# Performance work log

Hardware: AMD Instinct MI355X
Metric: run time of the kernel (lower is better)

## Reference

```python
import jax, jax.numpy as jnp
import numpy as np

MIN_DIST = 4
BASE_PRIMES = np.array([2, 3, 5, 7])  # A, C, G, U
# canonical pair prime products: AU=2*7=14, CG=3*5=15, GU=5*7=35


def nussinov(s):
    """Nussinov max-score non-crossing pairing: O(N^3) DP (vectorized per
    anti-diagonal) + stack-based traceback. s: [N,N] float64, symmetric, >=0.
    Returns symmetric 0/1 pair mask. Mirrors kirigami.nussinov (CPU numpy)."""
    N = s.shape[0]
    D = np.zeros((N, N))  # D[d, i] = dp[i, i+d]
    E = np.zeros((N, N))  # E[d, j] = dp[j-d, j]
    ar = np.arange(N)
    for d in range(1, N):
        m = N - d
        pair = (D[d - 2, 1:m + 1] if d >= 2 else 0.0) + s[ar[:m], ar[:m] + d]
        # split over k=i..j-1: dp[i,k] + dp[k+1,j] (k=i covers i-unpaired)
        split = (D[0:d, 0:m] + E[d - 1::-1, d:N]).max(axis=0)
        val = np.maximum(pair, split)
        D[d, :m] = val
        E[d, d:] = val
    dp = np.zeros((N, N))
    for d in range(1, N):
        dp[ar[:N - d], ar[:N - d] + d] = D[d, :N - d]
    eps = 1e-9
    pm = np.zeros((N, N))
    stack = [(0, N - 1)]
    while stack:
        i, j = stack.pop()
        if j <= i:
            continue
        v = dp[i, j]
        if v <= eps:
            continue
        if dp[i + 1, j] >= v - eps:
            stack.append((i + 1, j))
        elif s[i, j] > 0 and dp[i + 1, j - 1] + s[i, j] >= v - eps:
            pm[i, j] = pm[j, i] = 1.0
            stack.append((i + 1, j - 1))
        else:
            ks = np.arange(i, j)
            k = int(ks[np.argmax(dp[i, ks] + dp[ks + 1, j])])
            stack.append((i, k))
            stack.append((k + 1, j))
    return pm


def _premask(con, feat):
    """Symmetrize + remove sharp angles (tril(-4)+triu(4)) + canonical-pair mask."""
    c = con[0, 0]                      # [N, N]
    c = (c + c.T) * 0.5                # Symmetrize
    N = c.shape[0]
    idx = jnp.arange(N)
    dist_ok = jnp.abs(idx[:, None] - idx[None, :]) >= MIN_DIST  # RemoveSharp
    seq = feat[0, :4, :, 0]            # [4, N] one-hot base encoding
    primes = jnp.asarray(BASE_PRIMES)[jnp.argmax(seq, axis=0)]  # [N]
    prod = primes[:, None] * primes[None, :]
    canon = (prod == 14) | (prod == 15) | (prod == 35)          # Canonicalize
    return c * (dist_ok & canon)


def setup_inputs() -> dict:
    key = jax.random.key(0)
    k1, k2 = jax.random.split(key)
    N = 1024
    con = jax.random.uniform(k1, (1, 1, N, N), dtype=jnp.float32)
    feat = jax.random.normal(k2, (1, 16, N, N), dtype=jnp.float32)
    return {"con": con, "feat": feat}


def reference(con, feat):
    c = _premask(con, feat)
    # original: GPU->CPU numpy float64 DP, then mask back on device
    mask = nussinov(np.asarray(c, dtype=np.float64))
    out = c * jnp.asarray(mask, dtype=c.dtype)
    return out.reshape(con.shape)
```

## Files before the change

kernel.cpp:

```cpp
#include <hip/hip_runtime.h>

#define NN 1024
#define BT 32
#define TT 32
#define NTILES ((TT * (TT + 1)) / 2)

__device__ __forceinline__ double gload_cc(const double* p) {
    double v;
    asm volatile("global_load_dwordx2 %0, %1, off sc0 sc1" : "=v"(v) : "v"(p));
    return v;
}
__device__ __forceinline__ void gstore_cc(double* p, double v) {
    asm volatile("global_store_dwordx2 %0, %1, off sc0 sc1" :: "v"(p), "v"(v));
}
__device__ __forceinline__ void gstore_flag(int* p, int v) {
    asm volatile("global_store_dword %0, %1, off sc0 sc1" :: "v"(p), "v"(v));
}
#define VWAIT0 asm volatile("s_waitcnt vmcnt(0)" ::: "memory")

__device__ __forceinline__ void waitflag2(const int* f, int a0, int b0, int a1, int b1) {
    const int* p0 = &f[(a0 * TT + b0) << 4];
    const int* p1 = &f[(a1 * TT + b1) << 4];
    int it = 0;
    while (true) {
        int v0, v1;
        asm volatile("global_load_dword %0, %2, off sc0 sc1\n\t"
                     "global_load_dword %1, %3, off sc0 sc1\n\t"
                     "s_waitcnt vmcnt(0)"
                     : "=&v"(v0), "=&v"(v1)
                     : "v"(p0), "v"(p1));
        if (v0 & v1) break;
        if (it < 8) __builtin_amdgcn_s_sleep(1);
        else        __builtin_amdgcn_s_sleep(15);
        ++it;
    }
    asm volatile("" ::: "memory");
}
__device__ __forceinline__ void waitflag4(const int* f, int a0, int b0, int a1, int b1,
                                          int a2, int b2, int a3, int b3) {
    const int* p0 = &f[(a0 * TT + b0) << 4];
    const int* p1 = &f[(a1 * TT + b1) << 4];
    const int* p2 = &f[(a2 * TT + b2) << 4];
    const int* p3 = &f[(a3 * TT + b3) << 4];
    int it = 0;
    while (true) {
        int v0, v1, v2, v3;
        asm volatile("global_load_dword %0, %4, off sc0 sc1\n\t"
                     "global_load_dword %1, %5, off sc0 sc1\n\t"
                     "global_load_dword %2, %6, off sc0 sc1\n\t"
                     "global_load_dword %3, %7, off sc0 sc1\n\t"
                     "s_waitcnt vmcnt(0)"
                     : "=&v"(v0), "=&v"(v1), "=&v"(v2), "=&v"(v3)
                     : "v"(p0), "v"(p1), "v"(p2), "v"(p3));
        if (v0 & v1 & v2 & v3) break;
        if (it < 8) __builtin_amdgcn_s_sleep(1);
        else        __builtin_amdgcn_s_sleep(15);
        ++it;
    }
    asm volatile("" ::: "memory");
}
__device__ __forceinline__ void waitflag2_blk(const int* f, int a0, int b0, int a1, int b1) {
    if (threadIdx.x < 64) waitflag2(f, a0, b0, a1, b1);
    __syncthreads();
}
__device__ __forceinline__ void waitflag4_blk(const int* f, int a0, int b0, int a1, int b1,
                                              int a2, int b2, int a3, int b3) {
    if (threadIdx.x < 64) waitflag4(f, a0, b0, a1, b1, a2, b2, a3, b3);
    __syncthreads();
}

__global__ void primes_kernel(const float* __restrict__ feat, int* __restrict__ primes) {
    int i = blockIdx.x * blockDim.x + threadIdx.x;
    if (i < NN) {
        float best = feat[i * NN];
        int arg = 0;
        for (int ch = 1; ch < 4; ++ch) {
            float v = feat[ch * NN * NN + i * NN];
            if (v > best) { best = v; arg = ch; }
        }
        const int P[4] = {2, 3, 5, 7};
        primes[i] = P[arg];
    }
}

__global__ void prep_kernel(const float* __restrict__ con, const int* __restrict__ primes,
                            float* __restrict__ S, double* __restrict__ R,
                            double* __restrict__ C, float* __restrict__ out,
                            int* __restrict__ flags,
                            int* __restrict__ qi, int* __restrict__ qj,
                            int* __restrict__ qready, int* __restrict__ qctl) {
    int idx = blockIdx.x * blockDim.x + threadIdx.x;
    int i = idx >> 10;
    int j = idx & (NN - 1);
    float c = (con[idx] + con[j * NN + i]) * 0.5f;
    int prod = primes[i] * primes[j];
    bool canon = (prod == 14) | (prod == 15) | (prod == 35);
    int d = i - j; if (d < 0) d = -d;
    S[idx] = (canon && d >= 4) ? c : 0.0f;
    R[idx] = 0.0;
    C[idx] = 0.0;
    out[idx] = 0.0f;
    if (idx < TT * TT * 16) flags[idx] = 0;
    if (idx < 4096) qready[idx] = (idx == 0) ? 1 : 0;
    if (idx == 0) {
        qi[0] = 0; qj[0] = NN - 1;
        qctl[0] = 0;
        qctl[16] = 1;
        qctl[32] = 1;
    }
}

__global__ __launch_bounds__(256) void nuss_tiles_kernel(double* __restrict__ R,
                                                         double* __restrict__ C,
                                                         const float* __restrict__ S,
                                                         int* __restrict__ flags) {
    __shared__ double DJJc[32][33];
    __shared__ double Vtc[32][33];
    __shared__ __attribute__((aligned(16))) double Ast[32][34];
    __shared__ __attribute__((aligned(16))) double Bst[32][34];
    __shared__ double Pld[32][33];
    __shared__ float  Sld[32][32];
    __shared__ double edgeCol[33];

    int b = blockIdx.x, dd = 0;
    while (b >= TT - dd) { b -= TT - dd; ++dd; }
    const int I = b, J = b + dd;
    const int aI = I * BT, aJ = J * BT;
    const int tid = threadIdx.x;
    const int wid = tid >> 6;
    const int lane = tid & 63;
    const int r = lane >> 1;
    const int h = lane & 1;

    if (dd == 0) {
        #pragma unroll
        for (int w = 0; w < 4; ++w) {
            int idx = w * 256 + tid; int rr = idx >> 5, cc = idx & 31;
            Sld[rr][cc] = S[(aI + rr) * NN + aI + cc];
        }
        for (int idx = tid; idx < 32 * 33; idx += 256)
            ((double*)Vtc)[idx] = 0.0;
        __syncthreads();
        if (wid == 0) {
            double vrow[16];
            #pragma unroll
            for (int u = 0; u < 16; ++u) vrow[u] = 0.0;
            for (int s = 1; s <= 31; ++s) {
                int c = r + s;
                bool act = (c <= 31);
                double acc = 0.0;
                if (act) {
                    double t0 = 0.0, t1 = 0.0, t2 = 0.0, t3 = 0.0;
                    #pragma unroll
                    for (int u = 0; u < 16; u += 4) {
                        int k0 = h * 16 + u;
                        t0 = fmax(t0, vrow[u]     + Vtc[c][k0 + 1]);
                        t1 = fmax(t1, vrow[u + 1] + Vtc[c][k0 + 2]);
                        t2 = fmax(t2, vrow[u + 2] + Vtc[c][k0 + 3]);
                        t3 = fmax(t3, vrow[u + 3] + Vtc[c][k0 + 4]);
                    }
                    acc = fmax(fmax(t0, t1), fmax(t2, t3));
                }
                acc = fmax(acc, __shfl_xor(acc, 1));
                if (act) {
                    double best = fmax(acc, Vtc[c - 1][r + 1] + (double)Sld[r][c]);
                    if (h == 0) Vtc[c][r] = best;
                    #pragma unroll
                    for (int u = 0; u < 16; ++u)
                        if (h * 16 + u == c) vrow[u] = best;
                }
            }
        }
        __syncthreads();
        #pragma unroll
        for (int w = 0; w < 4; ++w) {
            int idx = w * 256 + tid; int rr = idx >> 5, cc = idx & 31;
            gstore_cc(&R[(aI + rr) * NN + aI + cc], Vtc[cc][rr]);
        }
        #pragma unroll
        for (int w = 0; w < 4; ++w) {
            int idx = w * 256 + tid; int cc = idx >> 5, rr = idx & 31;
            gstore_cc(&C[(aI + cc) * NN + aI + rr], Vtc[cc][rr]);
        }
        VWAIT0;
        __syncthreads();
        if (tid == 0) gstore_flag(&flags[(I * TT + I) << 4], 1);
        return;
    }

    const int nk = dd - 1;
    waitflag2_blk(flags, I, I, J, J);

    double ra[4], rb[4];
    double ec = 0.0, ve = 0.0;
    double asl[16];
    #pragma unroll
    for (int w = 0; w < 4; ++w) {
        int idx = w * 256 + tid; int cc = idx >> 5, mm = idx & 31;
        ra[w] = gload_cc(&C[(aJ + cc) * NN + aJ + mm]);
    }
    if (wid == 0) {
        #pragma unroll
        for (int u = 0; u < 16; ++u)
            asl[u] = gload_cc(&R[(aI + r) * NN + aI + h * 16 + u]);
        if (nk == 0) {
            if (lane < 33) ec = gload_cc(&R[(aI + lane) * NN + (aJ - 1)]);
            if (lane < 32) ve = gload_cc(&R[(aI + 32) * NN + aJ + lane]);
        }
    }
    #pragma unroll
    for (int w = 0; w < 4; ++w) {
        int idx = w * 256 + tid; int rr = idx >> 5, cc = idx & 31;
        Sld[rr][cc] = S[(aI + rr) * NN + aJ + cc];
    }
    for (int idx = tid; idx < 32 * 33; idx += 256)
        ((double*)Vtc)[idx] = 0.0;
    VWAIT0;
    #pragma unroll
    for (int w = 0; w < 4; ++w) {
        int idx = w * 256 + tid; int cc = idx >> 5, mm = idx & 31;
        DJJc[cc][mm] = ra[w];
    }
    if (tid < 32) DJJc[tid][32] = 0.0;
    double aslice[16];
    if (wid == 0) {
        #pragma unroll
        for (int u = 0; u < 16; ++u)
            aslice[u] = (h * 16 + u > r) ? asl[u] : -1.0e30;
    }
    __syncthreads();

    double P[16];
    #pragma unroll
    for (int x = 0; x < 16; ++x) P[x] = 0.0;
    const int rg = lane >> 3, cg = lane & 7;
    const int r4 = rg * 4, c4 = cg * 4;

    auto kkloop = [&]() {
        for (int kk = wid * 8; kk < wid * 8 + 8; ++kk) {
            double2 av0 = *(const double2*)&Ast[kk][r4];
            double2 av1 = *(const double2*)&Ast[kk][r4 + 2];
            double2 bv0 = *(const double2*)&Bst[kk][c4];
            double2 bv1 = *(const double2*)&Bst[kk][c4 + 2];
            P[0]  = fmax(P[0],  av0.x + bv0.x); P[1]  = fmax(P[1],  av0.x + bv0.y);
            P[2]  = fmax(P[2],  av0.x + bv1.x); P[3]  = fmax(P[3],  av0.x + bv1.y);
            P[4]  = fmax(P[4],  av0.y + bv0.x); P[5]  = fmax(P[5],  av0.y + bv0.y);
            P[6]  = fmax(P[6],  av0.y + bv1.x); P[7]  = fmax(P[7],  av0.y + bv1.y);
            P[8]  = fmax(P[8],  av1.x + bv0.x); P[9]  = fmax(P[9],  av1.x + bv0.y);
            P[10] = fmax(P[10], av1.x + bv1.x); P[11] = fmax(P[11], av1.x + bv1.y);
            P[12] = fmax(P[12], av1.y + bv0.x); P[13] = fmax(P[13], av1.y + bv0.y);
            P[14] = fmax(P[14], av1.y + bv1.x); P[15] = fmax(P[15], av1.y + bv1.y);
        }
    };
    auto proc = [&](int t1, int t2, bool last) {
        if (t2 >= 0) waitflag4_blk(flags, I, t1, t1, J, I, t2, t2, J);
        else         waitflag2_blk(flags, I, t1, t1, J);
        if (last && wid == 0) {
            if (lane < 33) ec = gload_cc(&R[(aI + lane) * NN + (aJ - 1)]);
            if (lane < 32) ve = gload_cc(&R[(aI + 32) * NN + aJ + lane]);
        }
        int k1 = t1 * BT;
        #pragma unroll
        for (int w = 0; w < 4; ++w) {
            int idx = w * 256 + tid; int rr = idx >> 5, kk = idx & 31;
            ra[w] = gload_cc(&R[(aI + rr) * NN + k1 + kk]);
            rb[w] = gload_cc(&C[(aJ + rr) * NN + k1 + 1 + kk]);
        }
        VWAIT0;
        #pragma unroll
        for (int w = 0; w < 4; ++w) {
            int idx = w * 256 + tid; int rr = idx >> 5, kk = idx & 31;
            Ast[kk][rr] = ra[w];
            Bst[kk][rr] = rb[w];
        }
        if (last && wid == 0) {
            if (lane < 33) edgeCol[lane] = ec;
            if (lane < 32) Vtc[lane][32] = ve;
        }
        __syncthreads();
        if (t2 >= 0) {
            int k2 = t2 * BT;
            #pragma unroll
            for (int w = 0; w < 4; ++w) {
                int idx = w * 256 + tid; int rr = idx >> 5, kk = idx & 31;
                ra[w] = gload_cc(&R[(aI + rr) * NN + k2 + kk]);
                rb[w] = gload_cc(&C[(aJ + rr) * NN + k2 + 1 + kk]);
            }
        }
        kkloop();
        if (t2 >= 0) {
            __syncthreads();
            VWAIT0;
            #pragma unroll
            for (int w = 0; w < 4; ++w) {
                int idx = w * 256 + tid; int rr = idx >> 5, kk = idx & 31;
                Ast[kk][rr] = ra[w];
                Bst[kk][rr] = rb[w];
            }
            __syncthreads();
            kkloop();
        }
        __syncthreads();
    };

    {
        int tl = (I + J) >> 1, tr = ((I + J) >> 1) + 1;
        int pend = -1;
        for (int q = 0; q < nk; ++q) {
            int t;
            if ((q & 1) == 0) { if (tl >= I + 1) t = tl--; else t = tr++; }
            else              { if (tr <= J - 1) t = tr++; else t = tl--; }
            if (pend < 0) { pend = t; continue; }
            int rp = (pend - I > J - pend) ? pend - I : J - pend;
            int rt = (t - I > J - t) ? t - I : J - t;
            if (rp == rt) { proc(pend, t, q == nk - 1); pend = -1; }
            else          { proc(pend, -1, false); pend = t; }
        }
        if (pend >= 0) proc(pend, -1, true);
    }

    if (nk > 0) {
        if (wid == 0) {
            #pragma unroll
            for (int x = 0; x < 4; ++x)
                #pragma unroll
                for (int y = 0; y < 4; ++y)
                    Pld[r4 + x][c4 + y] = P[x * 4 + y];
        }
        __syncthreads();
        if (wid == 1) {
            #pragma unroll
            for (int x = 0; x < 4; ++x)
                #pragma unroll
                for (int y = 0; y < 4; ++y)
                    Pld[r4 + x][c4 + y] = fmax(Pld[r4 + x][c4 + y], P[x * 4 + y]);
        }
        __syncthreads();
        if (wid == 2) {
            #pragma unroll
            for (int x = 0; x < 4; ++x)
                #pragma unroll
                for (int y = 0; y < 4; ++y)
                    Pld[r4 + x][c4 + y] = fmax(Pld[r4 + x][c4 + y], P[x * 4 + y]);
        }
        __syncthreads();
        if (wid == 3) {
            #pragma unroll
            for (int x = 0; x < 4; ++x)
                #pragma unroll
                for (int y = 0; y < 4; ++y)
                    Pld[r4 + x][c4 + y] = fmax(Pld[r4 + x][c4 + y], P[x * 4 + y]);
        }
        __syncthreads();
    } else {
        for (int idx = tid; idx < 32 * 33; idx += 256)
            ((double*)Pld)[idx] = 0.0;
        if (wid == 0) {
            if (lane < 33) edgeCol[lane] = ec;
            if (lane < 32) Vtc[lane][32] = ve;
        }
        __syncthreads();
    }

    if (wid == 0) {
        double vrow[16];
        #pragma unroll
        for (int u = 0; u < 16; ++u) vrow[u] = 0.0;

        double ecr = edgeCol[r];
        double ecp = edgeCol[r + 1];

        double tvA[16], qvA[16], tvB[16], qvB[16];
        double p1 = 0.0, shc = 0.0, shp = 0.0, erc = 0.0, erp = 0.0;

#define PREFB(TV, QV, SS)                                             \
    { int cc_ = (r + (SS) - 31) & 31;                                 \
      _Pragma("unroll")                                               \
      for (int u = 0; u < 16; ++u) {                                  \
          TV[u] = Vtc[cc_][h * 16 + u + 1];                           \
          QV[u] = DJJc[cc_][h * 16 + u + 1];                          \
      } }

#define STEPB(TV, QV, SS)                                             \
    { int c_ = r + (SS) - 31;                                         \
      bool act_ = ((unsigned)c_ < 32u);                               \
      int cc_ = c_ & 31;                                              \
      double er_  = Vtc[cc_][32];                                     \
      double dj0_ = DJJc[cc_][0];                                     \
      double pld_ = Pld[r][cc_];                                      \
      float  sld_ = Sld[r][cc_];                                      \
      shp = shc; erp = erc; erc = er_;                                \
      shc = __shfl_down(p1, 2);                                       \
      double acc_ = -1.0e30;                                          \
      if (act_) {                                                     \
          double t0_ = -1.0e30, t1_ = -1.0e30, t2_ = -1.0e30, t3_ = -1.0e30; \
          _Pragma("unroll")                                           \
          for (int u = 0; u < 16; u += 4) {                           \
              t0_ = fmax(t0_, aslice[u]     + TV[u]);                 \
              t1_ = fmax(t1_, aslice[u + 1] + TV[u + 1]);             \
              t2_ = fmax(t2_, aslice[u + 2] + TV[u + 2]);             \
              t3_ = fmax(t3_, aslice[u + 3] + TV[u + 3]);             \
          }                                                           \
          _Pragma("unroll")                                           \
          for (int u = 0; u < 16; u += 4) {                           \
              t0_ = fmax(t0_, vrow[u]     + QV[u]);                   \
              t1_ = fmax(t1_, vrow[u + 1] + QV[u + 1]);               \
              t2_ = fmax(t2_, vrow[u + 2] + QV[u + 2]);               \
              t3_ = fmax(t3_, vrow[u + 3] + QV[u + 3]);               \
          }                                                           \
          acc_ = fmax(fmax(t0_, t1_), fmax(t2_, t3_));                \
      }                                                               \
      acc_ = fmax(acc_, __shfl_xor(acc_, 1));                         \
      if (act_) {                                                     \
          double best_ = acc_;                                        \
          best_ = fmax(best_, (r == 31) ? erc : shc);                 \
          best_ = fmax(best_, ecr + dj0_);                            \
          best_ = fmax(best_, pld_);                                  \
          double pv_ = (c_ == 0) ? ecp : ((r == 31) ? erp : shp);     \
          best_ = fmax(best_, pv_ + (double)sld_);                    \
          if (h == 0) Vtc[c_][r] = best_;                             \
          _Pragma("unroll")                                           \
          for (int u = 0; u < 16; ++u)                                \
              if (h * 16 + u == c_) vrow[u] = best_;                  \
          p1 = best_;                                                 \
      } }

        PREFB(tvA, qvA, 0)
        for (int s2 = 0; s2 < 64; s2 += 2) {
            PREFB(tvB, qvB, s2 + 1)
            STEPB(tvA, qvA, s2)
            PREFB(tvA, qvA, s2 + 2)
            STEPB(tvB, qvB, s2 + 1)
        }
#undef PREFB
#undef STEPB
    }
    __syncthreads();

    #pragma unroll
    for (int w = 0; w < 4; ++w) {
        int idx = w * 256 + tid; int rr = idx >> 5, cc = idx & 31;
        gstore_cc(&R[(aI + rr) * NN + aJ + cc], Vtc[cc][rr]);
    }
    #pragma unroll
    for (int w = 0; w < 4; ++w) {
        int idx = w * 256 + tid; int cc = idx >> 5, rr = idx & 31;
        gstore_cc(&C[(aJ + cc) * NN + aI + rr], Vtc[cc][rr]);
    }
    VWAIT0;
    __syncthreads();
    if (tid == 0) gstore_flag(&flags[(I * TT + J) << 4], 1);
}

__global__ __launch_bounds__(256) void traceback_kernel(const double* __restrict__ R,
                                                        const double* __restrict__ C,
                                                        const float* __restrict__ S,
                                                        float* __restrict__ out,
                                                        int* __restrict__ qi,
                                                        int* __restrict__ qj,
                                                        int* __restrict__ qready,
                                                        int* __restrict__ qctl) {
    __shared__ double Rw[16][17];
    __shared__ float  Sw[16][17];
    __shared__ int sh_cmd, sh_i, sh_j;
    __shared__ double sred_v[4];
    __shared__ int sred_k[4];
    const double eps = 1e-9;
    const int tid = threadIdx.x;
    int* headp = qctl;
    int* tailp = qctl + 16;
    int* pendp = qctl + 32;

    int i = 0, j = 0; double v = 0.0;
    bool have = false;
    int ai = -(1 << 29), aj = 0;
    int myidx = -1;

    while (true) {
        if (tid == 0) {
            int cmd;
            int guard = 0;
            while (true) {
                if (!have) {
                    if (++guard > (1 << 22)) { cmd = -1; break; }
                    if (myidx < 0) myidx = atomicAdd(headp, 1);
                    int rdy = 0;
                    if (myidx < 4096)
                        rdy = __hip_atomic_load(&qready[myidx], __ATOMIC_RELAXED,
                                                __HIP_MEMORY_SCOPE_AGENT);
                    if (rdy) {
                        int ni, nj;
                        asm volatile("global_load_dword %0, %2, off sc0 sc1\n\t"
                                     "global_load_dword %1, %3, off sc0 sc1\n\t"
                                     "s_waitcnt vmcnt(0)"
                                     : "=&v"(ni), "=&v"(nj)
                                     : "v"(&qi[myidx]), "v"(&qj[myidx]));
                        myidx = -1;
                        i = ni; j = nj;
                        if (j <= i) { atomicAdd(pendp, -1); continue; }
                        v = R[i * NN + j];
                        if (v <= eps) { atomicAdd(pendp, -1); continue; }
                        have = true;
                        continue;
                    }
                    int pend = __hip_atomic_load(pendp, __ATOMIC_RELAXED,
                                                 __HIP_MEMORY_SCOPE_AGENT);
                    if (pend == 0) { cmd = -1; break; }
                    __builtin_amdgcn_s_sleep(2);
                    continue;
                }
                int u = i - ai, w = aj - j;
                if ((unsigned)u > 15u || (unsigned)w > 14u) { cmd = 1; break; }
                double a = Rw[u][w];
                if (a >= v - eps) {
                    ++i; v = a;
                    if (j <= i || v <= eps) { have = false; atomicAdd(pendp, -1); }
                    continue;
                }
                float sv = Sw[u][w];
                double b2 = Rw[u][w + 1];
                if (sv > 0.0f && b2 + (double)sv >= v - eps) {
                    out[i * NN + j] = sv; out[j * NN + i] = sv;
                    ++i; --j; v = b2;
                    if (j <= i || v <= eps) { have = false; atomicAdd(pendp, -1); }
                    continue;
                }
                cmd = 0; break;
            }
            sh_cmd = cmd; sh_i = i; sh_j = j;
        }
        __syncthreads();
        int cmd = sh_cmd;
        if (cmd < 0) break;

        if (cmd == 1) {
            int i0 = sh_i, j0 = sh_j;
            int di = tid >> 4, dj = tid & 15;
            int rr = i0 + 1 + di; if (rr > NN - 1) rr = NN - 1;
            int cc = j0 - dj;     if (cc < 0) cc = 0;
            Rw[di][dj] = R[rr * NN + cc];
            int sr = i0 + di;     if (sr > NN - 1) sr = NN - 1;
            Sw[di][dj] = S[sr * NN + cc];
            __syncthreads();
            if (tid == 0) { ai = i0; aj = j0; }
            continue;
        }

        const int si = sh_i, sj = sh_j;
        double bv = -1.0; int bk = 0x7fffffff;
        for (int k = si + tid; k < sj; k += 256) {
            double tv = R[si * NN + k] + C[sj * NN + k + 1];
            if (tv > bv) { bv = tv; bk = k; }
        }
        for (int off = 32; off; off >>= 1) {
            double ov = __shfl_down(bv, off);
            int    ok = __shfl_down(bk, off);
            if (ov > bv || (ov == bv && ok < bk)) { bv = ov; bk = ok; }
        }
        if ((tid & 63) == 0) { sred_v[tid >> 6] = bv; sred_k[tid >> 6] = bk; }
        __syncthreads();
        if (tid == 0) {
            double fv = sred_v[0]; int fk = sred_k[0];
            for (int w = 1; w < 4; ++w)
                if (sred_v[w] > fv || (sred_v[w] == fv && sred_k[w] < fk)) { fv = sred_v[w]; fk = sred_k[w]; }
            int slot = atomicAdd(tailp, 1);
            int rv = fk + 1;
            asm volatile("global_store_dword %0, %1, off sc0 sc1" :: "v"(&qi[slot]), "v"(rv));
            asm volatile("global_store_dword %0, %1, off sc0 sc1" :: "v"(&qj[slot]), "v"(sj));
            VWAIT0;
            atomicAdd(pendp, 1);
            VWAIT0;
            gstore_flag(&qready[slot], 1);
            j = fk;
            if (j <= i) { have = false; atomicAdd(pendp, -1); }
            else {
                v = R[i * NN + j];
                if (v <= eps) { have = false; atomicAdd(pendp, -1); }
                else have = true;
            }
        }
        __syncthreads();
    }
}

extern "C" void kernel_launch(void* const* d_in, const int* in_sizes, int n_in,
                              void* d_out, int out_size, void* d_ws, size_t ws_size,
                              hipStream_t stream) {
    const float* con  = (const float*)d_in[0];
    const float* feat = (const float*)d_in[1];
    float* out = (float*)d_out;

    char* ws = (char*)d_ws;
    double* R      = (double*)(ws);
    double* C      = (double*)(ws + (size_t)8  * 1024 * 1024);
    float*  S      = (float*) (ws + (size_t)16 * 1024 * 1024);
    int*    primes = (int*)   (ws + (size_t)20 * 1024 * 1024);
    int*    flags  = (int*)   (ws + (size_t)20 * 1024 * 1024 + 8192);
    char*   qbase  = ws + (size_t)20 * 1024 * 1024 + 128 * 1024;
    int*    qi     = (int*)(qbase);
    int*    qj     = (int*)(qbase + 16 * 1024);
    int*    qready = (int*)(qbase + 32 * 1024);
    int*    qctl   = (int*)(qbase + 48 * 1024);

    primes_kernel<<<(NN + 255) / 256, 256, 0, stream>>>(feat, primes);
    prep_kernel<<<(NN * NN) / 256, 256, 0, stream>>>(con, primes, S, R, C, out, flags,
                                                     qi, qj, qready, qctl);
    nuss_tiles_kernel<<<NTILES, 256, 0, stream>>>(R, C, S, flags);
    traceback_kernel<<<64, 256, 0, stream>>>(R, C, S, out, qi, qj, qready, qctl);
}
```

Before: 1.300 ms.

## Split tile wavefront recurrence across four waves with shared partial-max exchange

```diff
diff --git a/kernel.cpp b/kernel.cpp
--- a/kernel.cpp
+++ b/kernel.cpp
@@ -121,6 +121,7 @@
     __shared__ double Pld[32][33];
     __shared__ float  Sld[32][32];
     __shared__ double edgeCol[33];
+    __shared__ double Prt[2][4][32];
 
     int b = blockIdx.x, dd = 0;
     while (b >= TT - dd) { b -= TT - dd; ++dd; }
@@ -189,24 +190,27 @@
     }
 
     const int nk = dd - 1;
+    const int off = (wid & 1) * 16 + h * 8;
     waitflag2_blk(flags, I, I, J, J);
 
     double ra[4], rb[4];
     double ec = 0.0, ve = 0.0;
-    double asl[16];
+    double asl[8];
+    double ar1 = 0.0;
     #pragma unroll
     for (int w = 0; w < 4; ++w) {
         int idx = w * 256 + tid; int cc = idx >> 5, mm = idx & 31;
         ra[w] = gload_cc(&C[(aJ + cc) * NN + aJ + mm]);
     }
-    if (wid == 0) {
-        #pragma unroll
-        for (int u = 0; u < 16; ++u)
-            asl[u] = gload_cc(&R[(aI + r) * NN + aI + h * 16 + u]);
-        if (nk == 0) {
-            if (lane < 33) ec = gload_cc(&R[(aI + lane) * NN + (aJ - 1)]);
-            if (lane < 32) ve = gload_cc(&R[(aI + 32) * NN + aJ + lane]);
-        }
+    if (wid < 2) {
+        #pragma unroll
+        for (int u = 0; u < 8; ++u)
+            asl[u] = gload_cc(&R[(aI + r) * NN + aI + off + u]);
+    }
+    if (r < 31) ar1 = gload_cc(&R[(aI + r) * NN + aI + r + 1]);
+    if (wid == 0 && nk == 0) {
+        if (lane < 33) ec = gload_cc(&R[(aI + lane) * NN + (aJ - 1)]);
+        if (lane < 32) ve = gload_cc(&R[(aI + 32) * NN + aJ + lane]);
     }
     #pragma unroll
     for (int w = 0; w < 4; ++w) {
@@ -222,11 +226,18 @@
         DJJc[cc][mm] = ra[w];
     }
     if (tid < 32) DJJc[tid][32] = 0.0;
-    double aslice[16];
-    if (wid == 0) {
-        #pragma unroll
-        for (int u = 0; u < 16; ++u)
-            aslice[u] = (h * 16 + u > r) ? asl[u] : -1.0e30;
+    double slice8[8];
+    if (wid < 2) {
+        #pragma unroll
+        for (int u = 0; u < 8; ++u)
+            slice8[u] = (off + u > r + 1) ? asl[u] : -1.0e30;
+    } else {
+        #pragma unroll
+        for (int u = 0; u < 8; ++u) slice8[u] = 0.0;
+    }
+    if (wid == 0 && nk == 0) {
+        if (lane < 33) edgeCol[lane] = ec;
+        if (lane < 32) Vtc[lane][32] = ve;
     }
     __syncthreads();
 
@@ -355,85 +366,75 @@
     } else {
         for (int idx = tid; idx < 32 * 33; idx += 256)
             ((double*)Pld)[idx] = 0.0;
-        if (wid == 0) {
-            if (lane < 33) edgeCol[lane] = ec;
-            if (lane < 32) Vtc[lane][32] = ve;
-        }
-        __syncthreads();
-    }
-
-    if (wid == 0) {
-        double vrow[16];
-        #pragma unroll
-        for (int u = 0; u < 16; ++u) vrow[u] = 0.0;
-
+        __syncthreads();
+    }
+
+    {
+        const double* bsel = (wid < 2) ? &Vtc[0][0] : &DJJc[0][0];
         double ecr = edgeCol[r];
         double ecp = edgeCol[r + 1];
-
-        double tvA[16], qvA[16], tvB[16], qvB[16];
-        double p1 = 0.0, shc = 0.0, shp = 0.0, erc = 0.0, erp = 0.0;
-
-#define PREFB(TV, QV, SS)                                             \
-    { int cc_ = (r + (SS) - 31) & 31;                                 \
+        double pA[8], pB[8];
+        double p1 = 0.0, p2 = 0.0, shc = 0.0, shp = 0.0, erc = 0.0, erp = 0.0;
+
+#define PREFQ(PV, SS)                                                 \
+    { int cq_ = (r + (SS) - 31) & 31;                                 \
+      const double* bp_ = bsel + cq_ * 33 + off + 1;                  \
       _Pragma("unroll")                                               \
-      for (int u = 0; u < 16; ++u) {                                  \
-          TV[u] = Vtc[cc_][h * 16 + u + 1];                           \
-          QV[u] = DJJc[cc_][h * 16 + u + 1];                          \
-      } }
-
-#define STEPB(TV, QV, SS)                                             \
+      for (int u = 0; u < 8; ++u) PV[u] = bp_[u]; }
+
+#define STEPQ(PV, SS, BUF)                                            \
     { int c_ = r + (SS) - 31;                                         \
       bool act_ = ((unsigned)c_ < 32u);                               \
       int cc_ = c_ & 31;                                              \
+      double t0_ = fmax(slice8[0] + PV[0], slice8[1] + PV[1]);        \
+      double t1_ = fmax(slice8[2] + PV[2], slice8[3] + PV[3]);        \
+      double t2_ = fmax(slice8[4] + PV[4], slice8[5] + PV[5]);        \
+      double t3_ = fmax(slice8[6] + PV[6], slice8[7] + PV[7]);        \
+      double pa_ = fmax(fmax(t0_, t1_), fmax(t2_, t3_));              \
+      pa_ = fmax(pa_, __shfl_xor(pa_, 1));                            \
+      if (h == 0) Prt[BUF][wid][r] = pa_;                             \
+      __syncthreads();                                                \
+      double a0_ = Prt[BUF][0][r];                                    \
+      double a1_ = Prt[BUF][1][r];                                    \
+      double a2_ = Prt[BUF][2][r];                                    \
+      double a3_ = Prt[BUF][3][r];                                    \
       double er_  = Vtc[cc_][32];                                     \
       double dj0_ = DJJc[cc_][0];                                     \
       double pld_ = Pld[r][cc_];                                      \
       float  sld_ = Sld[r][cc_];                                      \
       shp = shc; erp = erc; erc = er_;                                \
       shc = __shfl_down(p1, 2);                                       \
-      double acc_ = -1.0e30;                                          \
-      if (act_) {                                                     \
-          double t0_ = -1.0e30, t1_ = -1.0e30, t2_ = -1.0e30, t3_ = -1.0e30; \
-          _Pragma("unroll")                                           \
-          for (int u = 0; u < 16; u += 4) {                           \
-              t0_ = fmax(t0_, aslice[u]     + TV[u]);                 \
-              t1_ = fmax(t1_, aslice[u + 1] + TV[u + 1]);             \
-              t2_ = fmax(t2_, aslice[u + 2] + TV[u + 2]);             \
-              t3_ = fmax(t3_, aslice[u + 3] + TV[u + 3]);             \
-          }                                                           \
-          _Pragma("unroll")                                           \
-          for (int u = 0; u < 16; u += 4) {                           \
-              t0_ = fmax(t0_, vrow[u]     + QV[u]);                   \
-              t1_ = fmax(t1_, vrow[u + 1] + QV[u + 1]);               \
-              t2_ = fmax(t2_, vrow[u + 2] + QV[u + 2]);               \
-              t3_ = fmax(t3_, vrow[u + 3] + QV[u + 3]);               \
-          }                                                           \
-          acc_ = fmax(fmax(t0_, t1_), fmax(t2_, t3_));                \
-      }                                                               \
-      acc_ = fmax(acc_, __shfl_xor(acc_, 1));                         \
+      double shd_ = __shfl_down(p2, 4);                               \
+      p2 = p1;                                                        \
+      double acc_ = fmax(fmax(a0_, a1_), fmax(a2_, a3_));             \
       if (act_) {                                                     \
           double best_ = acc_;                                        \
           best_ = fmax(best_, (r == 31) ? erc : shc);                 \
+          if (r < 31)                                                 \
+              best_ = fmax(best_, ar1 + ((r == 30) ? erc : shd_));    \
           best_ = fmax(best_, ecr + dj0_);                            \
           best_ = fmax(best_, pld_);                                  \
           double pv_ = (c_ == 0) ? ecp : ((r == 31) ? erp : shp);     \
           best_ = fmax(best_, pv_ + (double)sld_);                    \
-          if (h == 0) Vtc[c_][r] = best_;                             \
-          _Pragma("unroll")                                           \
-          for (int u = 0; u < 16; ++u)                                \
-              if (h * 16 + u == c_) vrow[u] = best_;                  \
+          if (wid == 0 && h == 0) Vtc[c_][r] = best_;                 \
+          if (wid >= 2) {                                             \
+              _Pragma("unroll")                                       \
+              for (int u = 0; u < 8; ++u)                             \
+                  if (off + u == c_) slice8[u] = best_;               \
+          }                                                           \
           p1 = best_;                                                 \
       } }
 
-        PREFB(tvA, qvA, 0)
+        PREFQ(pA, 0)
+        PREFQ(pB, 1)
         for (int s2 = 0; s2 < 64; s2 += 2) {
-            PREFB(tvB, qvB, s2 + 1)
-            STEPB(tvA, qvA, s2)
-            PREFB(tvA, qvA, s2 + 2)
-            STEPB(tvB, qvB, s2 + 1)
-        }
-#undef PREFB
-#undef STEPB
+            STEPQ(pA, s2, 0)
+            PREFQ(pA, s2 + 2)
+            STEPQ(pB, s2 + 1, 1)
+            PREFQ(pB, s2 + 3)
+        }
+#undef PREFQ
+#undef STEPQ
     }
     __syncthreads();
 
@@ -552,9 +553,9 @@
             double tv = R[si * NN + k] + C[sj * NN + k + 1];
             if (tv > bv) { bv = tv; bk = k; }
         }
-        for (int off = 32; off; off >>= 1) {
-            double ov = __shfl_down(bv, off);
-            int    ok = __shfl_down(bk, off);
+        for (int offr = 32; offr; offr >>= 1) {
+            double ov = __shfl_down(bv, offr);
+            int    ok = __shfl_down(bk, offr);
             if (ov > bv || (ov == bv && ok < bk)) { bv = ov; bk = ok; }
         }
         if ((tid & 63) == 0) { sred_v[tid >> 6] = bv; sred_k[tid >> 6] = bk; }
```

Result: faster. 1.141 ms (median of 2 runs) (-12.2%).
